# Kernel optimization log

Measured on AMD Instinct MI355X. Metric: run time of the kernel, lower is better.

Reference implementation:

```python
import jax, jax.numpy as jnp
import numpy as np

B, T, E, H, L = 16, 1024, 1024, 512, 6
C = 1024  # conv out channels


def _lstm_dir(x_tbi, Wih, Whh, bih, bhh):
    # x_tbi: [T, B, I]; single-direction LSTM, PyTorch gate order (i, f, g, o)
    Bn = x_tbi.shape[1]
    Hh = Whh.shape[1]
    b = bih + bhh
    def step(carry, xt):
        h, c = carry
        g = xt @ Wih.T + h @ Whh.T + b  # [B, 4H]
        i, f, gg, o = jnp.split(g, 4, axis=-1)
        c = jax.nn.sigmoid(f) * c + jax.nn.sigmoid(i) * jnp.tanh(gg)
        h = jax.nn.sigmoid(o) * jnp.tanh(c)
        return (h, c), h
    h0 = jnp.zeros((Bn, Hh), x_tbi.dtype)
    _, hs = jax.lax.scan(step, (h0, h0), x_tbi)
    return hs  # [T, B, H]


def _forward(embeddings, attention_mask, labels, conv_w, conv_b, bn_gamma, bn_beta,
             bn_mean, bn_var, lstm_Wih, lstm_Whh, lstm_bih, lstm_bhh,
             cls_w, cls_b, crf_start, crf_end, crf_trans):
    # Conv1d(E->1024, k=5, pad=2) on [B, C, T]
    x = jax.lax.conv_general_dilated(
        embeddings.astype(jnp.float32).transpose(0, 2, 1), conv_w,
        window_strides=(1,), padding=[(2, 2)],
        dimension_numbers=("NCH", "OIH", "NCH")) + conv_b[None, :, None]
    # BatchNorm1d (eval: running stats) fused + ReLU
    scale = bn_gamma / jnp.sqrt(bn_var + 1e-5)
    x = jax.nn.relu(x * scale[None, :, None] + (bn_beta - bn_mean * scale)[None, :, None])
    # time-major for the LSTM scans: [T, B, 1024]
    x = x.transpose(2, 0, 1)
    for l in range(3):
        fw = _lstm_dir(x, lstm_Wih[l, 0], lstm_Whh[l, 0], lstm_bih[l, 0], lstm_bhh[l, 0])
        bw = _lstm_dir(x[::-1], lstm_Wih[l, 1], lstm_Whh[l, 1], lstm_bih[l, 1], lstm_bhh[l, 1])[::-1]
        x = jnp.concatenate([fw, bw], axis=-1)  # [T, B, 2H]
    logits = x @ cls_w.T + cls_b  # [T, B, L]; dropout is identity in eval
    # CRF negative log-likelihood (torchcrf, batch_first handled by time-major layout)
    mask = (attention_mask.astype(bool) & (labels != -100)).T  # [T, B]
    tags = jnp.where(labels == -100, 0, labels).astype(jnp.int32).T  # [T, B]
    mf = mask.astype(logits.dtype)
    bidx = jnp.arange(logits.shape[1])
    # numerator: score of the given tag sequence
    score0 = crf_start[tags[0]] + logits[0, bidx, tags[0]]
    def num_step(carry, inp):
        score, prev = carry
        et, mt, mtf, tt = inp
        s = crf_trans[prev, tt] + et[bidx, tt]
        return (score + mtf * s, jnp.where(mt, tt, prev)), None
    (num, last), _ = jax.lax.scan(
        num_step, (score0, tags[0]), (logits[1:], mask[1:], mf[1:], tags[1:]))
    num = num + crf_end[last]
    # denominator: forward algorithm (log partition)
    def den_step(alpha, inp):
        et, mt = inp
        nxt = jax.nn.logsumexp(alpha[:, :, None] + crf_trans[None, :, :] + et[:, None, :], axis=1)
        return jnp.where(mt[:, None], nxt, alpha), None
    alpha, _ = jax.lax.scan(den_step, crf_start + logits[0], (logits[1:], mask[1:]))
    den = jax.nn.logsumexp(alpha + crf_end, axis=-1)
    return -(num - den).mean()  # reduction='mean' over batch, negated


def setup_inputs() -> dict:
    key = jax.random.key(0)
    ks = jax.random.split(key, 16)
    p = lambda k, shp: jax.random.normal(k, shp, jnp.float32) * 0.05
    return {
        "embeddings": jax.random.normal(ks[0], (B, T, E), jnp.float32),
        "attention_mask": jnp.ones((B, T), jnp.int32),
        "labels": jax.random.randint(ks[1], (B, T), 0, L, jnp.int32),
        "conv_w": p(ks[2], (C, E, 5)),
        "conv_b": p(ks[3], (C,)),
        "bn_gamma": jnp.ones((C,), jnp.float32),
        "bn_beta": jnp.zeros((C,), jnp.float32),
        "bn_mean": p(ks[4], (C,)),
        "bn_var": jax.random.uniform(ks[5], (C,), jnp.float32, 0.5, 1.5),
        "lstm_Wih": p(ks[6], (3, 2, 4 * H, C)),
        "lstm_Whh": p(ks[7], (3, 2, 4 * H, H)),
        "lstm_bih": p(ks[8], (3, 2, 4 * H)),
        "lstm_bhh": p(ks[9], (3, 2, 4 * H)),
        "cls_w": p(ks[10], (L, 2 * H)),
        "cls_b": p(ks[11], (L,)),
        "crf_start": p(ks[12], (L,)),
        "crf_end": p(ks[13], (L,)),
        "crf_trans": p(ks[14], (L, L)),
    }


def reference(embeddings, attention_mask, labels, conv_w, conv_b, bn_gamma, bn_beta,
              bn_mean, bn_var, lstm_Wih, lstm_Whh, lstm_bih, lstm_bhh,
              cls_w, cls_b, crf_start, crf_end, crf_trans):
    return _forward(embeddings, attention_mask, labels, conv_w, conv_b, bn_gamma,
                    bn_beta, bn_mean, bn_var, lstm_Wih, lstm_Whh, lstm_bih,
                    lstm_bhh, cls_w, cls_b, crf_start, crf_end, crf_trans)
```

## Files before the change

### kernel.cpp

```cpp
#include <hip/hip_runtime.h>


typedef short bf16_t;
typedef __attribute__((ext_vector_type(8))) short bf16x8;
typedef __attribute__((ext_vector_type(4))) float f32x4;

__device__ __forceinline__ bf16_t f2b(float x) {
  unsigned u = __float_as_uint(x);
  unsigned r = (u + 0x7fffu + ((u >> 16) & 1u)) >> 16;
  return (bf16_t)(unsigned short)r;
}
__device__ __forceinline__ float b2f(bf16_t b) {
  return __uint_as_float(((unsigned)(unsigned short)b) << 16);
}
__device__ __forceinline__ float blo(unsigned u) { return __uint_as_float(u << 16); }
__device__ __forceinline__ float bhi(unsigned u) { return __uint_as_float(u & 0xffff0000u); }


__global__ void embed_pad_k(const float* __restrict__ E, bf16_t* __restrict__ P) {
  size_t i4 = ((size_t)blockIdx.x * 256 + threadIdx.x) * 4;
  if (i4 >= 16ul * 1028 * 1024) return;
  int e = (int)(i4 & 1023);
  size_t rest = i4 >> 10;
  int tp = (int)(rest % 1028);
  int b  = (int)(rest / 1028);
  bf16_t o[4];
  if (tp >= 2 && tp < 1026) {
    const float4 v = *(const float4*)(E + (((size_t)b * 1024 + (tp - 2)) * 1024 + e));
    o[0] = f2b(v.x); o[1] = f2b(v.y); o[2] = f2b(v.z); o[3] = f2b(v.w);
  } else {
    o[0] = o[1] = o[2] = o[3] = 0;
  }
  *(uint2*)(P + i4) = *(const uint2*)o;
}

__global__ void convw_cvt_k(const float* __restrict__ S, bf16_t* __restrict__ D) {
  int idx = blockIdx.x * 256 + threadIdx.x;
  if (idx >= 1024 * 1024) return;
  int c = idx >> 10, e = idx & 1023;
  const float* s = S + (size_t)idx * 5;
#pragma unroll
  for (int kk = 0; kk < 5; kk++) D[(size_t)c * 5120 + kk * 1024 + e] = f2b(s[kk]);
}

__global__ void bnfold_k(const float* cb, const float* g, const float* be,
                         const float* mn, const float* vr, float* a, float* dd) {
  int c = blockIdx.x * 256 + threadIdx.x;
  if (c < 1024) {
    float s = g[c] * rsqrtf(vr[c] + 1e-5f);
    a[c] = s;
    dd[c] = (cb[c] - mn[c]) * s + be[c];
  }
}

__global__ void wihcvt_k(const float* __restrict__ S, bf16_t* __restrict__ D) {
  size_t i = ((size_t)blockIdx.x * 256 + threadIdx.x) * 4;
  if (i >= 3ul * 2 * 2048 * 1024) return;
  float4 v = *(const float4*)(S + i);
  bf16_t o[4] = {f2b(v.x), f2b(v.y), f2b(v.z), f2b(v.w)};
  *(uint2*)(D + i) = *(const uint2*)o;
}

__global__ __launch_bounds__(256, 1) void gemm_gates(
    const bf16_t* __restrict__ A, const bf16_t* __restrict__ W,
    const float* __restrict__ bias0, const float* __restrict__ bias1,
    bf16_t* __restrict__ G) {
  const int tid = threadIdx.x;
  const int m0 = (blockIdx.x >> 4) * 128, n0 = (blockIdx.x & 15) * 128;
  __shared__ bf16_t As[128][72];
  __shared__ bf16_t Bs[128][72];
  const int wv = tid >> 6, ln = tid & 63;
  const int wm = (wv >> 1) * 64, wn = (wv & 1) * 64;
  const int lb = ln & 15, lq = ln >> 4;
  f32x4 acc[4][4] = {};
  for (int k0 = 0; k0 < 1024; k0 += 64) {
    __syncthreads();
#pragma unroll
    for (int i = 0; i < 4; i++) {
      int idx = tid + i * 256, r = idx >> 3, ch = idx & 7;
      *(uint4*)&As[r][ch * 8] = *(const uint4*)(A + (size_t)(m0 + r) * 1024 + k0 + ch * 8);
      *(uint4*)&Bs[r][ch * 8] = *(const uint4*)(W + (size_t)(n0 + r) * 1024 + k0 + ch * 8);
    }
    __syncthreads();
#pragma unroll
    for (int kk = 0; kk < 2; kk++) {
      bf16x8 af[4], bfr[4];
#pragma unroll
      for (int t = 0; t < 4; t++) {
        af[t]  = *(const bf16x8*)&As[wm + t * 16 + lb][kk * 32 + lq * 8];
        bfr[t] = *(const bf16x8*)&Bs[wn + t * 16 + lb][kk * 32 + lq * 8];
      }
#pragma unroll
      for (int mt = 0; mt < 4; mt++)
#pragma unroll
        for (int nt = 0; nt < 4; nt++)
          acc[mt][nt] = __builtin_amdgcn_mfma_f32_16x16x32_bf16(af[mt], bfr[nt], acc[mt][nt], 0, 0, 0);
    }
  }
#pragma unroll
  for (int mt = 0; mt < 4; mt++)
#pragma unroll
    for (int nt = 0; nt < 4; nt++) {
      int col = n0 + wn + nt * 16 + lb;
      int g = col >> 9, j = col & 511;
      int jb2 = j >> 4, jp = j & 15;
      float bs = bias0[col] + bias1[col];
      int row0 = m0 + wm + mt * 16;
      int t = row0 >> 4;
      bf16_t tmp[4];
#pragma unroll
      for (int r = 0; r < 4; r++) tmp[r] = f2b(acc[mt][nt][r] + bs);
      size_t base = (((size_t)t * 32 + jb2) * 4 + g) * 256 + jp * 16 + lq * 4;
      *(uint2*)&G[base] = *(const uint2*)tmp;
    }
}

__global__ __launch_bounds__(256, 1) void conv_gemm(
    const bf16_t* __restrict__ EP, const bf16_t* __restrict__ Wc,
    const float* __restrict__ bn_a, const float* __restrict__ bn_d,
    bf16_t* __restrict__ X) {
  const int tid = threadIdx.x;
  const int m0 = (blockIdx.x >> 3) * 128, n0 = (blockIdx.x & 7) * 128;
  __shared__ bf16_t As[128][72];
  __shared__ bf16_t Bs[128][72];
  const int wv = tid >> 6, ln = tid & 63;
  const int wm = (wv >> 1) * 64, wn = (wv & 1) * 64;
  const int lb = ln & 15, lq = ln >> 4;
  f32x4 acc[4][4] = {};
  for (int kk = 0; kk < 5; kk++) {
    for (int k0 = 0; k0 < 1024; k0 += 64) {
      __syncthreads();
#pragma unroll
      for (int i = 0; i < 4; i++) {
        int idx = tid + i * 256, r = idx >> 3, ch = idx & 7;
        int m = m0 + r;
        const bf16_t* ap = EP + ((size_t)((m & 15) * 1028 + (m >> 4) + kk)) * 1024 + k0 + ch * 8;
        *(uint4*)&As[r][ch * 8] = *(const uint4*)ap;
        *(uint4*)&Bs[r][ch * 8] = *(const uint4*)(Wc + (size_t)(n0 + r) * 5120 + kk * 1024 + k0 + ch * 8);
      }
      __syncthreads();
#pragma unroll
      for (int kq = 0; kq < 2; kq++) {
        bf16x8 af[4], bfr[4];
#pragma unroll
        for (int t = 0; t < 4; t++) {
          af[t]  = *(const bf16x8*)&As[wm + t * 16 + lb][kq * 32 + lq * 8];
          bfr[t] = *(const bf16x8*)&Bs[wn + t * 16 + lb][kq * 32 + lq * 8];
        }
#pragma unroll
        for (int mt = 0; mt < 4; mt++)
#pragma unroll
          for (int nt = 0; nt < 4; nt++)
            acc[mt][nt] = __builtin_amdgcn_mfma_f32_16x16x32_bf16(af[mt], bfr[nt], acc[mt][nt], 0, 0, 0);
      }
    }
  }
#pragma unroll
  for (int mt = 0; mt < 4; mt++)
#pragma unroll
    for (int nt = 0; nt < 4; nt++) {
      int col = n0 + wn + nt * 16 + lb;
      float sa = bn_a[col], sd = bn_d[col];
#pragma unroll
      for (int r = 0; r < 4; r++) {
        int row = m0 + wm + mt * 16 + lq * 4 + r;
        float v = fmaxf(acc[mt][nt][r] * sa + sd, 0.f);
        X[(size_t)row * 1024 + col] = f2b(v);
      }
    }
}

__global__ __launch_bounds__(256, 1) void rec_kernel(
    const float* __restrict__ Whh,
    const bf16_t* __restrict__ Gfw,
    const bf16_t* __restrict__ Gbw,
    bf16_t* __restrict__ xout,
    unsigned long long* __restrict__ hstT,
    float* __restrict__ cst,
    int t0f, int t0b, int nsteps, int tag_base) {
  const int tid = threadIdx.x;
  const int d  = blockIdx.x >> 5;
  const int j0 = (blockIdx.x & 31) << 4;
  const int wv = tid >> 6;
  const int ln = tid & 63;
  const int lb = ln & 15;
  const int lq = ln >> 4;

  __shared__ bf16_t Hb[16][522];
  __shared__ float  Ex[4][16][17];
  __shared__ bf16_t Gs[2][1024];
  __shared__ bf16_t XB[16][16][16];

  bf16x8 afrag[16];
  {
    const float* wrow = Whh + ((size_t)(d * 2048 + wv * 512 + j0 + lb)) * 512;
#pragma unroll
    for (int kk = 0; kk < 16; kk++) {
      const float* wp = wrow + kk * 32 + lq * 8;
      float4 va = *(const float4*)wp;
      float4 vb = *(const float4*)(wp + 4);
      bf16x8 fr;
      fr[0] = f2b(va.x); fr[1] = f2b(va.y); fr[2] = f2b(va.z); fr[3] = f2b(va.w);
      fr[4] = f2b(vb.x); fr[5] = f2b(vb.y); fr[6] = f2b(vb.z); fr[7] = f2b(vb.w);
      afrag[kk] = fr;
    }
  }
  const int cb = tid & 15;
  const int cj = tid >> 4;
  float creg = cst[((size_t)d * 16 + cb) * 512 + j0 + cj];
  const bf16_t* G = (d == 0) ? Gfw : Gbw;
  const int jblk = j0 >> 4;

  {
    const int trow = (d == 0) ? 0 : (nsteps - 1);
    uint2 g0 = *(const uint2*)(G + ((size_t)trow * 32 + jblk) * 1024 + tid * 4);
    *(uint2*)&Gs[0][tid * 4] = g0;
  }

  for (int s = 0; s < nsteps; s++) {
    const int rb = (s & 1) ^ 1, wb = s & 1;
    const int t = (d == 0) ? (t0f + s) : (t0b + nsteps - 1 - s);
    uint2 gnext = {0, 0};
    if (s + 1 < nsteps) {
      const int trn = (d == 0) ? (s + 1) : (nsteps - 2 - s);
      gnext = *(const uint2*)(G + ((size_t)trn * 32 + jblk) * 1024 + tid * 4);
    }
    {
      const unsigned long long* src =
          hstT + ((size_t)rb * 2 + d) * 4096 + (wv << 10);
      const unsigned expect = (unsigned)(tag_base + s);
      unsigned long long v[16];
      bool ok;
      do {
        ok = true;
#pragma unroll
        for (int i = 0; i < 16; i++)
          v[i] = __hip_atomic_load(src + i * 64 + ln, __ATOMIC_RELAXED, __HIP_MEMORY_SCOPE_AGENT);
#pragma unroll
        for (int i = 0; i < 16; i++) ok = ok && ((unsigned)(v[i] >> 32) == expect);
      } while (!__all(ok));
#pragma unroll
      for (int i = 0; i < 16; i++) {
        int pair = (wv << 6) + i * 4 + lq;
        *(unsigned*)&Hb[lb][pair * 2] = (unsigned)v[i];
      }
    }
    __syncthreads();
    f32x4 acc0 = {}, acc1 = {};
#pragma unroll
    for (int kk = 0; kk < 8; kk++) {
      bf16x8 b0 = *(const bf16x8*)&Hb[lb][(2 * kk) * 32 + lq * 8];
      bf16x8 b1 = *(const bf16x8*)&Hb[lb][(2 * kk + 1) * 32 + lq * 8];
      acc0 = __builtin_amdgcn_mfma_f32_16x16x32_bf16(afrag[2 * kk], b0, acc0, 0, 0, 0);
      acc1 = __builtin_amdgcn_mfma_f32_16x16x32_bf16(afrag[2 * kk + 1], b1, acc1, 0, 0, 0);
    }
#pragma unroll
    for (int r = 0; r < 4; r++) Ex[wv][lq * 4 + r][lb] = acc0[r] + acc1[r];
    __syncthreads();
    const bf16_t* gs = &Gs[s & 1][0];
    float gi = Ex[0][cj][cb] + b2f(gs[0 * 256 + cj * 16 + cb]);
    float gf = Ex[1][cj][cb] + b2f(gs[1 * 256 + cj * 16 + cb]);
    float gg = Ex[2][cj][cb] + b2f(gs[2 * 256 + cj * 16 + cb]);
    float go = Ex[3][cj][cb] + b2f(gs[3 * 256 + cj * 16 + cb]);
    float si = 1.f / (1.f + expf(-gi));
    float sf = 1.f / (1.f + expf(-gf));
    float so = 1.f / (1.f + expf(-go));
    creg = sf * creg + si * tanhf(gg);
    float h = so * tanhf(creg);
    bf16_t hb = f2b(h);
    XB[t & 15][cb][cj] = hb;
    if (s + 1 < nsteps) *(uint2*)&Gs[(s + 1) & 1][tid * 4] = gnext;
    {
      unsigned hu = (unsigned)(unsigned short)hb;
      unsigned hp = (unsigned)__shfl_down((int)hu, 16, 64);
      if ((cj & 1) == 0) {
        unsigned data = hu | (hp << 16);
        unsigned long long val =
            ((unsigned long long)(unsigned)(tag_base + s + 1) << 32) | data;
        unsigned long long* dst =
            hstT + ((size_t)wb * 2 + d) * 4096 + (size_t)((j0 + cj) >> 1) * 16 + cb;
        __hip_atomic_store(dst, val, __ATOMIC_RELAXED, __HIP_MEMORY_SCOPE_AGENT);
      }
    }
    if ((s & 15) == 15) {
      __syncthreads();
      const int tbase = (d == 0) ? (t - 15) : t;
      const int tt = tbase + (tid >> 4);
      const int b  = tid & 15;
      const bf16_t* xb = &XB[tid >> 4][b][0];
      bf16_t* xo = xout + ((size_t)tt * 16 + b) * 1024 + d * 512 + j0;
      *(uint4*)xo = *(const uint4*)xb;
      *(uint4*)(xo + 8) = *(const uint4*)(xb + 8);
    }
  }
  cst[((size_t)d * 16 + cb) * 512 + j0 + cj] = creg;
}

__global__ void cls_kernel(const bf16_t* __restrict__ X, const float* __restrict__ Wc,
                           const float* __restrict__ bc, float* __restrict__ Lg) {
  int wv = threadIdx.x >> 6, ln = threadIdx.x & 63;
  size_t m = (size_t)blockIdx.x * 4 + wv;
  const bf16_t* xr = X + m * 1024 + ln * 16;
  uint4 v0 = *(const uint4*)xr;
  uint4 v1 = *(const uint4*)(xr + 8);
  float xv[16];
  const unsigned* p0 = (const unsigned*)&v0;
  const unsigned* p1 = (const unsigned*)&v1;
#pragma unroll
  for (int i = 0; i < 4; i++) { xv[2 * i] = blo(p0[i]); xv[2 * i + 1] = bhi(p0[i]); }
#pragma unroll
  for (int i = 0; i < 4; i++) { xv[8 + 2 * i] = blo(p1[i]); xv[8 + 2 * i + 1] = bhi(p1[i]); }
#pragma unroll
  for (int l = 0; l < 6; l++) {
    const float* wr = Wc + l * 1024 + ln * 16;
    float p = 0.f;
#pragma unroll
    for (int i = 0; i < 16; i++) p += xv[i] * wr[i];
#pragma unroll
    for (int off = 32; off; off >>= 1) p += __shfl_xor(p, off, 64);
    if (ln == 0) Lg[m * 6 + l] = p + bc[l];
  }
}

__global__ void crf_kernel(const float* __restrict__ Lg, const int* __restrict__ attn,
                           const int* __restrict__ labels, const float* __restrict__ start,
                           const float* __restrict__ endw, const float* __restrict__ trans,
                           float* __restrict__ out) {
  int b = blockIdx.x, ln = threadIdx.x;
  __shared__ float str[36];
  __shared__ int tg[1024];
  __shared__ unsigned char mk[1024];
  if (ln < 36) str[ln] = trans[ln];
  for (int t = ln; t < 1024; t += 64) {
    int lab = labels[b * 1024 + t];
    mk[t] = (unsigned char)((attn[b * 1024 + t] != 0) && (lab != -100));
    tg[t] = (lab == -100) ? 0 : lab;
  }
  __syncthreads();
  int j = ln;
  bool act = j < 6;
  float alpha = act ? (start[j] + Lg[(size_t)b * 6 + j]) : -1e30f;
  for (int t = 1; t < 1024; t++) {
    float vv[6], mx = -1e30f;
#pragma unroll
    for (int i = 0; i < 6; i++) {
      float ai = __shfl(alpha, i, 64);
      float v = ai + str[i * 6 + (act ? j : 0)];
      vv[i] = v;
      mx = fmaxf(mx, v);
    }
    float sm = 0.f;
#pragma unroll
    for (int i = 0; i < 6; i++) sm += expf(vv[i] - mx);
    float na = mx + logf(sm) + (act ? Lg[((size_t)t * 16 + b) * 6 + j] : 0.f);
    if (mk[t] && act) alpha = na;
  }
  float z = act ? (alpha + endw[j]) : -1e30f;
  float zm = z;
#pragma unroll
  for (int i = 0; i < 6; i++) zm = fmaxf(zm, __shfl(z, i, 64));
  float zs = act ? expf(z - zm) : 0.f;
  float tot = 0.f;
#pragma unroll
  for (int i = 0; i < 6; i++) tot += __shfl(zs, i, 64);
  float den = zm + logf(tot);
  if (ln == 0) {
    float score = start[tg[0]] + Lg[(size_t)b * 6 + tg[0]];
    int prev = tg[0];
    for (int t = 1; t < 1024; t++) {
      if (mk[t]) {
        score += str[prev * 6 + tg[t]] + Lg[((size_t)t * 16 + b) * 6 + tg[t]];
        prev = tg[t];
      }
    }
    score += endw[prev];
    atomicAdd(out, (den - score) * (1.0f / 16.0f));
  }
}

extern "C" void kernel_launch(void* const* d_in, const int* in_sizes, int n_in,
                              void* d_out, int out_size, void* d_ws, size_t ws_size,
                              hipStream_t stream) {
  const float* emb    = (const float*)d_in[0];
  const int*   attn   = (const int*)d_in[1];
  const int*   labels = (const int*)d_in[2];
  const float* convw  = (const float*)d_in[3];
  const float* convb  = (const float*)d_in[4];
  const float* bng    = (const float*)d_in[5];
  const float* bnb    = (const float*)d_in[6];
  const float* bnm    = (const float*)d_in[7];
  const float* bnv    = (const float*)d_in[8];
  const float* wih    = (const float*)d_in[9];
  const float* whh    = (const float*)d_in[10];
  const float* bih    = (const float*)d_in[11];
  const float* bhh    = (const float*)d_in[12];
  const float* clsw   = (const float*)d_in[13];
  const float* clsb   = (const float*)d_in[14];
  const float* crfs   = (const float*)d_in[15];
  const float* crfe   = (const float*)d_in[16];
  const float* crft   = (const float*)d_in[17];
  (void)in_sizes; (void)n_in; (void)out_size; (void)ws_size;

  char* w = (char*)d_ws;
  auto alloc = [&](size_t bytes) { char* p = w; w += (bytes + 255) & ~(size_t)255; return p; };
  bf16_t* emb_pad = (bf16_t*)alloc(16ul * 1028 * 1024 * 2);
  bf16_t* wconv   = (bf16_t*)alloc(1024ul * 5120 * 2);
  float*  bn_a    = (float*)alloc(4096);
  float*  bn_d    = (float*)alloc(4096);
  bf16_t* wihb    = (bf16_t*)alloc(3ul * 2 * 2048 * 1024 * 2);
  bf16_t* xA      = (bf16_t*)alloc(16384ul * 1024 * 2);
  bf16_t* xB      = (bf16_t*)alloc(16384ul * 1024 * 2);
  bf16_t* gfw     = (bf16_t*)alloc(512ul * 32 * 1024 * 2);
  bf16_t* gbw     = (bf16_t*)alloc(512ul * 32 * 1024 * 2);
  unsigned long long* hstT = (unsigned long long*)alloc(2ul * 2 * 4096 * 8);
  float*  cst     = (float*)alloc(2ul * 16 * 512 * 4);
  float*  lgt     = (float*)alloc(16384ul * 6 * 4);

  hipMemsetAsync(d_out, 0, 4, stream);

  embed_pad_k<<<16448, 256, 0, stream>>>(emb, emb_pad);
  convw_cvt_k<<<4096, 256, 0, stream>>>(convw, wconv);
  bnfold_k<<<4, 256, 0, stream>>>(convb, bng, bnb, bnm, bnv, bn_a, bn_d);
  wihcvt_k<<<12288, 256, 0, stream>>>(wih, wihb);

  conv_gemm<<<128 * 8, 256, 0, stream>>>(emb_pad, wconv, bn_a, bn_d, xA);

  bf16_t* xin = xA;
  bf16_t* xout = xB;
  for (int l = 0; l < 3; l++) {
    hipMemsetAsync(hstT, 0, 2ul * 2 * 4096 * 8, stream);
    hipMemsetAsync(cst, 0, 2ul * 16 * 512 * 4, stream);
    for (int c = 0; c < 2; c++) {
      int t0f = c * 512, t0b = (1 - c) * 512;
      gemm_gates<<<64 * 16, 256, 0, stream>>>(
          xin + (size_t)t0f * 16 * 1024, wihb + ((size_t)l * 2 + 0) * 2048 * 1024,
          bih + (l * 2 + 0) * 2048, bhh + (l * 2 + 0) * 2048, gfw);
      gemm_gates<<<64 * 16, 256, 0, stream>>>(
          xin + (size_t)t0b * 16 * 1024, wihb + ((size_t)l * 2 + 1) * 2048 * 1024,
          bih + (l * 2 + 1) * 2048, bhh + (l * 2 + 1) * 2048, gbw);
      rec_kernel<<<64, 256, 0, stream>>>(whh + (size_t)l * 2 * 2048 * 512,
                                         gfw, gbw, xout, hstT, cst, t0f, t0b, 512, c * 512);
    }
    bf16_t* tmp = xin; xin = xout; xout = tmp;
  }

  cls_kernel<<<4096, 256, 0, stream>>>(xin, clsw, clsb, lgt);
  crf_kernel<<<16, 64, 0, stream>>>(lgt, attn, labels, crfs, crfe, crft, (float*)d_out);
}
```

Baseline: 8.985 ms.

## Consolidate LSTM recurrence into 16 larger blocks covering 64 units each

The persistent recurrence kernel moves from 64 workgroups of 256 threads, each owning 16 hidden units, to 16 workgroups of 512 threads, each owning 64 hidden units per direction. Each wave now holds two 16-row weight fragments and reuses every loaded h fragment for two MFMAs. Each thread computes two cell states. The aim is to cut the number of blocks that poll and broadcast hidden state through global memory every timestep, which lowers sync contention and redundant h reads. In exchange, each block does more MFMA and gate work per step on fewer CUs, which lengthens the per-step critical path inside a block.

```diff
diff --git a/kernel.cpp b/kernel.cpp
--- a/kernel.cpp
+++ b/kernel.cpp
@@ -170,7 +170,7 @@
     }
 }
 
-__global__ __launch_bounds__(256, 1) void rec_kernel(
+__global__ __launch_bounds__(512, 1) void rec_kernel(
     const float* __restrict__ Whh,
     const bf16_t* __restrict__ Gfw,
     const bf16_t* __restrict__ Gbw,
@@ -179,21 +179,25 @@
     float* __restrict__ cst,
     int t0f, int t0b, int nsteps, int tag_base) {
   const int tid = threadIdx.x;
-  const int d  = blockIdx.x >> 5;
-  const int j0 = (blockIdx.x & 31) << 4;
+  const int d  = blockIdx.x & 1;
+  const int wg = blockIdx.x >> 1;
+  const int j0 = wg << 6;
   const int wv = tid >> 6;
   const int ln = tid & 63;
   const int lb = ln & 15;
   const int lq = ln >> 4;
+  const int gate = wv & 3;
+  const int u0 = (wv >> 2) << 5;
 
   __shared__ bf16_t Hb[16][522];
-  __shared__ float  Ex[4][16][17];
-  __shared__ bf16_t Gs[2][1024];
-  __shared__ bf16_t XB[16][16][16];
-
-  bf16x8 afrag[16];
-  {
-    const float* wrow = Whh + ((size_t)(d * 2048 + wv * 512 + j0 + lb)) * 512;
+  __shared__ float  Ex[4][64][17];
+  __shared__ bf16_t Gs[2][4096];
+  __shared__ bf16_t XB[16][16][72];
+
+  bf16x8 afrag[2][16];
+#pragma unroll
+  for (int nt = 0; nt < 2; nt++) {
+    const float* wrow = Whh + ((size_t)(d * 2048 + gate * 512 + j0 + u0 + nt * 16 + lb)) * 512;
 #pragma unroll
     for (int kk = 0; kk < 16; kk++) {
       const float* wp = wrow + kk * 32 + lq * 8;
@@ -202,98 +206,122 @@
       bf16x8 fr;
       fr[0] = f2b(va.x); fr[1] = f2b(va.y); fr[2] = f2b(va.z); fr[3] = f2b(va.w);
       fr[4] = f2b(vb.x); fr[5] = f2b(vb.y); fr[6] = f2b(vb.z); fr[7] = f2b(vb.w);
-      afrag[kk] = fr;
+      afrag[nt][kk] = fr;
     }
   }
   const int cb = tid & 15;
-  const int cj = tid >> 4;
-  float creg = cst[((size_t)d * 16 + cb) * 512 + j0 + cj];
+  const int cu = tid >> 4;
+  float creg0 = cst[((size_t)d * 16 + cb) * 512 + j0 + cu];
+  float creg1 = cst[((size_t)d * 16 + cb) * 512 + j0 + cu + 32];
   const bf16_t* G = (d == 0) ? Gfw : Gbw;
-  const int jblk = j0 >> 4;
+  const int jb0 = j0 >> 4;
+  const int gc  = tid >> 7;
+  const int go  = tid & 127;
 
   {
     const int trow = (d == 0) ? 0 : (nsteps - 1);
-    uint2 g0 = *(const uint2*)(G + ((size_t)trow * 32 + jblk) * 1024 + tid * 4);
-    *(uint2*)&Gs[0][tid * 4] = g0;
+    *(uint4*)&Gs[0][gc * 1024 + go * 8] =
+        *(const uint4*)(G + ((size_t)trow * 32 + jb0 + gc) * 1024 + go * 8);
   }
 
   for (int s = 0; s < nsteps; s++) {
     const int rb = (s & 1) ^ 1, wb = s & 1;
     const int t = (d == 0) ? (t0f + s) : (t0b + nsteps - 1 - s);
-    uint2 gnext = {0, 0};
+    uint4 gnext = {0, 0, 0, 0};
     if (s + 1 < nsteps) {
       const int trn = (d == 0) ? (s + 1) : (nsteps - 2 - s);
-      gnext = *(const uint2*)(G + ((size_t)trn * 32 + jblk) * 1024 + tid * 4);
+      gnext = *(const uint4*)(G + ((size_t)trn * 32 + jb0 + gc) * 1024 + go * 8);
     }
     {
-      const unsigned long long* src =
-          hstT + ((size_t)rb * 2 + d) * 4096 + (wv << 10);
+      const unsigned long long* src = hstT + ((size_t)rb * 2 + d) * 4096;
       const unsigned expect = (unsigned)(tag_base + s);
-      unsigned long long v[16];
+      unsigned long long v[8];
       bool ok;
       do {
         ok = true;
 #pragma unroll
-        for (int i = 0; i < 16; i++)
-          v[i] = __hip_atomic_load(src + i * 64 + ln, __ATOMIC_RELAXED, __HIP_MEMORY_SCOPE_AGENT);
-#pragma unroll
-        for (int i = 0; i < 16; i++) ok = ok && ((unsigned)(v[i] >> 32) == expect);
+        for (int i = 0; i < 8; i++)
+          v[i] = __hip_atomic_load(src + i * 512 + tid, __ATOMIC_RELAXED, __HIP_MEMORY_SCOPE_AGENT);
+#pragma unroll
+        for (int i = 0; i < 8; i++) ok = ok && ((unsigned)(v[i] >> 32) == expect);
       } while (!__all(ok));
 #pragma unroll
-      for (int i = 0; i < 16; i++) {
-        int pair = (wv << 6) + i * 4 + lq;
-        *(unsigned*)&Hb[lb][pair * 2] = (unsigned)v[i];
+      for (int i = 0; i < 8; i++) {
+        int q = i * 512 + tid;
+        *(unsigned*)&Hb[q & 15][(q >> 4) * 2] = (unsigned)v[i];
       }
     }
     __syncthreads();
     f32x4 acc0 = {}, acc1 = {};
 #pragma unroll
-    for (int kk = 0; kk < 8; kk++) {
-      bf16x8 b0 = *(const bf16x8*)&Hb[lb][(2 * kk) * 32 + lq * 8];
-      bf16x8 b1 = *(const bf16x8*)&Hb[lb][(2 * kk + 1) * 32 + lq * 8];
-      acc0 = __builtin_amdgcn_mfma_f32_16x16x32_bf16(afrag[2 * kk], b0, acc0, 0, 0, 0);
-      acc1 = __builtin_amdgcn_mfma_f32_16x16x32_bf16(afrag[2 * kk + 1], b1, acc1, 0, 0, 0);
-    }
-#pragma unroll
-    for (int r = 0; r < 4; r++) Ex[wv][lq * 4 + r][lb] = acc0[r] + acc1[r];
+    for (int kk = 0; kk < 16; kk++) {
+      bf16x8 b = *(const bf16x8*)&Hb[lb][kk * 32 + lq * 8];
+      acc0 = __builtin_amdgcn_mfma_f32_16x16x32_bf16(afrag[0][kk], b, acc0, 0, 0, 0);
+      acc1 = __builtin_amdgcn_mfma_f32_16x16x32_bf16(afrag[1][kk], b, acc1, 0, 0, 0);
+    }
+#pragma unroll
+    for (int r = 0; r < 4; r++) {
+      Ex[gate][u0 + lq * 4 + r][lb]      = acc0[r];
+      Ex[gate][u0 + 16 + lq * 4 + r][lb] = acc1[r];
+    }
     __syncthreads();
-    const bf16_t* gs = &Gs[s & 1][0];
-    float gi = Ex[0][cj][cb] + b2f(gs[0 * 256 + cj * 16 + cb]);
-    float gf = Ex[1][cj][cb] + b2f(gs[1 * 256 + cj * 16 + cb]);
-    float gg = Ex[2][cj][cb] + b2f(gs[2 * 256 + cj * 16 + cb]);
-    float go = Ex[3][cj][cb] + b2f(gs[3 * 256 + cj * 16 + cb]);
-    float si = 1.f / (1.f + expf(-gi));
-    float sf = 1.f / (1.f + expf(-gf));
-    float so = 1.f / (1.f + expf(-go));
-    creg = sf * creg + si * tanhf(gg);
-    float h = so * tanhf(creg);
-    bf16_t hb = f2b(h);
-    XB[t & 15][cb][cj] = hb;
-    if (s + 1 < nsteps) *(uint2*)&Gs[(s + 1) & 1][tid * 4] = gnext;
     {
-      unsigned hu = (unsigned)(unsigned short)hb;
-      unsigned hp = (unsigned)__shfl_down((int)hu, 16, 64);
-      if ((cj & 1) == 0) {
-        unsigned data = hu | (hp << 16);
-        unsigned long long val =
-            ((unsigned long long)(unsigned)(tag_base + s + 1) << 32) | data;
+      const bf16_t* gs = &Gs[s & 1][0];
+      const int uA = cu, uB = cu + 32;
+      const bf16_t* gA = gs + (uA >> 4) * 1024 + (uA & 15) * 16 + cb;
+      const bf16_t* gB = gs + (uB >> 4) * 1024 + (uB & 15) * 16 + cb;
+      float giA = Ex[0][uA][cb] + b2f(gA[0]);
+      float gfA = Ex[1][uA][cb] + b2f(gA[256]);
+      float ggA = Ex[2][uA][cb] + b2f(gA[512]);
+      float goA = Ex[3][uA][cb] + b2f(gA[768]);
+      float giB = Ex[0][uB][cb] + b2f(gB[0]);
+      float gfB = Ex[1][uB][cb] + b2f(gB[256]);
+      float ggB = Ex[2][uB][cb] + b2f(gB[512]);
+      float goB = Ex[3][uB][cb] + b2f(gB[768]);
+      float siA = 1.f / (1.f + expf(-giA));
+      float sfA = 1.f / (1.f + expf(-gfA));
+      float soA = 1.f / (1.f + expf(-goA));
+      float siB = 1.f / (1.f + expf(-giB));
+      float sfB = 1.f / (1.f + expf(-gfB));
+      float soB = 1.f / (1.f + expf(-goB));
+      creg0 = sfA * creg0 + siA * tanhf(ggA);
+      creg1 = sfB * creg1 + siB * tanhf(ggB);
+      float hA = soA * tanhf(creg0);
+      float hB = soB * tanhf(creg1);
+      bf16_t hbA = f2b(hA), hbB = f2b(hB);
+      XB[t & 15][cb][uA] = hbA;
+      XB[t & 15][cb][uB] = hbB;
+      if (s + 1 < nsteps) *(uint4*)&Gs[(s + 1) & 1][gc * 1024 + go * 8] = gnext;
+      unsigned h0 = (unsigned)(unsigned short)hbA;
+      unsigned h1 = (unsigned)(unsigned short)hbB;
+      unsigned p0 = (unsigned)__shfl_down((int)h0, 16, 64);
+      unsigned p1 = (unsigned)__shfl_down((int)h1, 16, 64);
+      if ((cu & 1) == 0) {
+        unsigned long long tagv =
+            ((unsigned long long)(unsigned)(tag_base + s + 1)) << 32;
         unsigned long long* dst =
-            hstT + ((size_t)wb * 2 + d) * 4096 + (size_t)((j0 + cj) >> 1) * 16 + cb;
-        __hip_atomic_store(dst, val, __ATOMIC_RELAXED, __HIP_MEMORY_SCOPE_AGENT);
+            hstT + ((size_t)wb * 2 + d) * 4096 + (size_t)((j0 + cu) >> 1) * 16 + cb;
+        __hip_atomic_store(dst, tagv | (unsigned long long)(h0 | (p0 << 16)),
+                           __ATOMIC_RELAXED, __HIP_MEMORY_SCOPE_AGENT);
+        __hip_atomic_store(dst + 256, tagv | (unsigned long long)(h1 | (p1 << 16)),
+                           __ATOMIC_RELAXED, __HIP_MEMORY_SCOPE_AGENT);
       }
     }
     if ((s & 15) == 15) {
       __syncthreads();
       const int tbase = (d == 0) ? (t - 15) : t;
-      const int tt = tbase + (tid >> 4);
-      const int b  = tid & 15;
-      const bf16_t* xb = &XB[tid >> 4][b][0];
-      bf16_t* xo = xout + ((size_t)tt * 16 + b) * 1024 + d * 512 + j0;
-      *(uint4*)xo = *(const uint4*)xb;
-      *(uint4*)(xo + 8) = *(const uint4*)(xb + 8);
-    }
-  }
-  cst[((size_t)d * 16 + cb) * 512 + j0 + cj] = creg;
+      const int row = tid >> 1, half = tid & 1;
+      const int tp = row >> 4, b = row & 15;
+      const bf16_t* xb = &XB[tp][b][half * 32];
+      bf16_t* xo = xout + ((size_t)(tbase + tp) * 16 + b) * 1024 + d * 512 + j0 + half * 32;
+      *(uint4*)(xo)      = *(const uint4*)(xb);
+      *(uint4*)(xo + 8)  = *(const uint4*)(xb + 8);
+      *(uint4*)(xo + 16) = *(const uint4*)(xb + 16);
+      *(uint4*)(xo + 24) = *(const uint4*)(xb + 24);
+    }
+  }
+  cst[((size_t)d * 16 + cb) * 512 + j0 + cu]      = creg0;
+  cst[((size_t)d * 16 + cb) * 512 + j0 + cu + 32] = creg1;
 }
 
 __global__ void cls_kernel(const bf16_t* __restrict__ X, const float* __restrict__ Wc,
@@ -438,7 +466,7 @@
       gemm_gates<<<64 * 16, 256, 0, stream>>>(
           xin + (size_t)t0b * 16 * 1024, wihb + ((size_t)l * 2 + 1) * 2048 * 1024,
           bih + (l * 2 + 1) * 2048, bhh + (l * 2 + 1) * 2048, gbw);
-      rec_kernel<<<64, 256, 0, stream>>>(whh + (size_t)l * 2 * 2048 * 512,
+      rec_kernel<<<16, 512, 0, stream>>>(whh + (size_t)l * 2 * 2048 * 512,
                                          gfw, gbw, xout, hstT, cst, t0f, t0b, 512, c * 512);
     }
     bf16_t* tmp = xin; xin = xout; xout = tmp;
```

New measurement: 12.58 ms. 40.0% more time.

## Overlap second-half input-gate GEMMs with first-half recurrence in one fused launch

Applied to the files above, without the earlier changes.

Moves shared memory into a common buffer so the recurrence and the gate GEMM can share one kernel. Each layer now launches a fused kernel: 64 blocks run the first 512-step recurrence while the other 2048 blocks compute the gate pre-activations for the second half, written into double buffers (one reuses emb_pad). This is meant to hide the gate GEMM behind the latency-bound recurrence, which only occupies 64 CUs. The risk is that the GEMM blocks compete with the persistent recurrence blocks for memory bandwidth and CU scheduling. The recurrence blocks must also be resident together for their cross-block sync, and the launch depends on them being dispatched first.

```diff
diff --git a/kernel.cpp b/kernel.cpp
--- a/kernel.cpp
+++ b/kernel.cpp
@@ -61,14 +61,15 @@
   *(uint2*)(D + i) = *(const uint2*)o;
 }
 
-__global__ __launch_bounds__(256, 1) void gemm_gates(
+__device__ __forceinline__ void gemm_gates_body(
+    char* smem, int blk,
     const bf16_t* __restrict__ A, const bf16_t* __restrict__ W,
     const float* __restrict__ bias0, const float* __restrict__ bias1,
     bf16_t* __restrict__ G) {
   const int tid = threadIdx.x;
-  const int m0 = (blockIdx.x >> 4) * 128, n0 = (blockIdx.x & 15) * 128;
-  __shared__ bf16_t As[128][72];
-  __shared__ bf16_t Bs[128][72];
+  const int m0 = (blk >> 4) * 128, n0 = (blk & 15) * 128;
+  bf16_t (*As)[72] = (bf16_t(*)[72])smem;
+  bf16_t (*Bs)[72] = (bf16_t(*)[72])(smem + 18432);
   const int wv = tid >> 6, ln = tid & 63;
   const int wm = (wv >> 1) * 64, wn = (wv & 1) * 64;
   const int lb = ln & 15, lq = ln >> 4;
@@ -170,7 +171,8 @@
     }
 }
 
-__global__ __launch_bounds__(256, 1) void rec_kernel(
+__device__ __forceinline__ void rec_body(
+    char* smem, int blk,
     const float* __restrict__ Whh,
     const bf16_t* __restrict__ Gfw,
     const bf16_t* __restrict__ Gbw,
@@ -179,17 +181,17 @@
     float* __restrict__ cst,
     int t0f, int t0b, int nsteps, int tag_base) {
   const int tid = threadIdx.x;
-  const int d  = blockIdx.x >> 5;
-  const int j0 = (blockIdx.x & 31) << 4;
+  const int d  = blk >> 5;
+  const int j0 = (blk & 31) << 4;
   const int wv = tid >> 6;
   const int ln = tid & 63;
   const int lb = ln & 15;
   const int lq = ln >> 4;
 
-  __shared__ bf16_t Hb[16][522];
-  __shared__ float  Ex[4][16][17];
-  __shared__ bf16_t Gs[2][1024];
-  __shared__ bf16_t XB[16][16][16];
+  bf16_t (*Hb)[522]     = (bf16_t(*)[522])smem;
+  float  (*Ex)[16][17]  = (float(*)[16][17])(smem + 16704);
+  bf16_t (*Gs)[1024]    = (bf16_t(*)[1024])(smem + 21056);
+  bf16_t (*XB)[16][16]  = (bf16_t(*)[16][16])(smem + 25152);
 
   bf16x8 afrag[16];
   {
@@ -296,6 +298,44 @@
   cst[((size_t)d * 16 + cb) * 512 + j0 + cj] = creg;
 }
 
+__global__ __launch_bounds__(256, 1) void gemm_gates(
+    const bf16_t* __restrict__ A, const bf16_t* __restrict__ W,
+    const float* __restrict__ bias0, const float* __restrict__ bias1,
+    bf16_t* __restrict__ G) {
+  __shared__ __align__(16) char smem[36864];
+  gemm_gates_body(smem, blockIdx.x, A, W, bias0, bias1, G);
+}
+
+__global__ __launch_bounds__(256, 1) void rec_kernel(
+    const float* __restrict__ Whh, const bf16_t* __restrict__ Gfw,
+    const bf16_t* __restrict__ Gbw, bf16_t* __restrict__ xout,
+    unsigned long long* __restrict__ hstT, float* __restrict__ cst,
+    int t0f, int t0b, int nsteps, int tag_base) {
+  __shared__ __align__(16) char smem[36864];
+  rec_body(smem, blockIdx.x, Whh, Gfw, Gbw, xout, hstT, cst, t0f, t0b, nsteps, tag_base);
+}
+
+__global__ __launch_bounds__(256, 1) void rec_gates_fused(
+    const float* __restrict__ Whh, const bf16_t* __restrict__ Gfw,
+    const bf16_t* __restrict__ Gbw, bf16_t* __restrict__ xout,
+    unsigned long long* __restrict__ hstT, float* __restrict__ cst,
+    int t0f, int t0b, int nsteps, int tag_base,
+    const bf16_t* __restrict__ A2f, const bf16_t* __restrict__ W2f,
+    const float* __restrict__ b0f, const float* __restrict__ b1f,
+    bf16_t* __restrict__ G2f,
+    const bf16_t* __restrict__ A2b, const bf16_t* __restrict__ W2b,
+    const float* __restrict__ b0b, const float* __restrict__ b1b,
+    bf16_t* __restrict__ G2b) {
+  __shared__ __align__(16) char smem[36864];
+  if (blockIdx.x < 64) {
+    rec_body(smem, blockIdx.x, Whh, Gfw, Gbw, xout, hstT, cst, t0f, t0b, nsteps, tag_base);
+  } else {
+    int gb = blockIdx.x - 64;
+    if (gb < 1024) gemm_gates_body(smem, gb, A2f, W2f, b0f, b1f, G2f);
+    else           gemm_gates_body(smem, gb - 1024, A2b, W2b, b0b, b1b, G2b);
+  }
+}
+
 __global__ void cls_kernel(const bf16_t* __restrict__ X, const float* __restrict__ Wc,
                            const float* __restrict__ bc, float* __restrict__ Lg) {
   int wv = threadIdx.x >> 6, ln = threadIdx.x & 63;
@@ -410,8 +450,10 @@
   bf16_t* wihb    = (bf16_t*)alloc(3ul * 2 * 2048 * 1024 * 2);
   bf16_t* xA      = (bf16_t*)alloc(16384ul * 1024 * 2);
   bf16_t* xB      = (bf16_t*)alloc(16384ul * 1024 * 2);
-  bf16_t* gfw     = (bf16_t*)alloc(512ul * 32 * 1024 * 2);
-  bf16_t* gbw     = (bf16_t*)alloc(512ul * 32 * 1024 * 2);
+  bf16_t* gfw0    = (bf16_t*)alloc(512ul * 32 * 1024 * 2);
+  bf16_t* gbw0    = (bf16_t*)alloc(512ul * 32 * 1024 * 2);
+  bf16_t* gbw1    = (bf16_t*)alloc(512ul * 32 * 1024 * 2);
+  bf16_t* gfw1    = emb_pad;
   unsigned long long* hstT = (unsigned long long*)alloc(2ul * 2 * 4096 * 8);
   float*  cst     = (float*)alloc(2ul * 16 * 512 * 4);
   float*  lgt     = (float*)alloc(16384ul * 6 * 4);
@@ -430,17 +472,18 @@
   for (int l = 0; l < 3; l++) {
     hipMemsetAsync(hstT, 0, 2ul * 2 * 4096 * 8, stream);
     hipMemsetAsync(cst, 0, 2ul * 16 * 512 * 4, stream);
-    for (int c = 0; c < 2; c++) {
-      int t0f = c * 512, t0b = (1 - c) * 512;
-      gemm_gates<<<64 * 16, 256, 0, stream>>>(
-          xin + (size_t)t0f * 16 * 1024, wihb + ((size_t)l * 2 + 0) * 2048 * 1024,
-          bih + (l * 2 + 0) * 2048, bhh + (l * 2 + 0) * 2048, gfw);
-      gemm_gates<<<64 * 16, 256, 0, stream>>>(
-          xin + (size_t)t0b * 16 * 1024, wihb + ((size_t)l * 2 + 1) * 2048 * 1024,
-          bih + (l * 2 + 1) * 2048, bhh + (l * 2 + 1) * 2048, gbw);
-      rec_kernel<<<64, 256, 0, stream>>>(whh + (size_t)l * 2 * 2048 * 512,
-                                         gfw, gbw, xout, hstT, cst, t0f, t0b, 512, c * 512);
-    }
+    const bf16_t* wih_f = wihb + ((size_t)l * 2 + 0) * 2048 * 1024;
+    const bf16_t* wih_b = wihb + ((size_t)l * 2 + 1) * 2048 * 1024;
+    const float* bih_f = bih + (l * 2 + 0) * 2048, *bhh_f = bhh + (l * 2 + 0) * 2048;
+    const float* bih_b = bih + (l * 2 + 1) * 2048, *bhh_b = bhh + (l * 2 + 1) * 2048;
+    const float* whh_l = whh + (size_t)l * 2 * 2048 * 512;
+    gemm_gates<<<1024, 256, 0, stream>>>(xin, wih_f, bih_f, bhh_f, gfw0);
+    gemm_gates<<<1024, 256, 0, stream>>>(xin + 512ul * 16 * 1024, wih_b, bih_b, bhh_b, gbw0);
+    rec_gates_fused<<<64 + 2048, 256, 0, stream>>>(
+        whh_l, gfw0, gbw0, xout, hstT, cst, 0, 512, 512, 0,
+        xin + 512ul * 16 * 1024, wih_f, bih_f, bhh_f, gfw1,
+        xin,                     wih_b, bih_b, bhh_b, gbw1);
+    rec_kernel<<<64, 256, 0, stream>>>(whh_l, gfw1, gbw1, xout, hstT, cst, 512, 0, 512, 512);
     bf16_t* tmp = xin; xin = xout; xout = tmp;
   }
 
```

Result: slower. 12.80 ms (+42.5%).
